# Kernel tuning notes

Measured on AMD Instinct MI355X. Metric: run time of the kernel, lower is better.

The kernel has to match this reference:

```python
import jax, jax.numpy as jnp
import numpy as np

N_HEADS = 16

def setup_inputs() -> dict:
    key = jax.random.key(0)
    ks = jax.random.split(key, 5)
    b, t, k = 2, 2048, 1024
    x = jax.random.normal(ks[0], (b, t, k), dtype=jnp.float32)
    Wq = jax.random.normal(ks[1], (k, k), dtype=jnp.float32) * 0.02
    Wk = jax.random.normal(ks[2], (k, k), dtype=jnp.float32) * 0.02
    Wv = jax.random.normal(ks[3], (k, k), dtype=jnp.float32) * 0.02
    Wo = jax.random.normal(ks[4], (k, k), dtype=jnp.float32) * 0.02
    return {"x": x, "Wq": Wq, "Wk": Wk, "Wv": Wv, "Wo": Wo}

def reference(x, Wq, Wk, Wv, Wo):
    b, t, k = x.shape
    h = N_HEADS
    hs = k // h
    # torch nn.Linear(k, k, bias=False): y = x @ W.T
    Q = (x @ Wq.T).reshape(b, t, h, hs).transpose(0, 2, 1, 3)  # [b,h,t,hs]
    K = (x @ Wk.T).reshape(b, t, h, hs).transpose(0, 2, 1, 3)
    V = (x @ Wv.T).reshape(b, t, h, hs).transpose(0, 2, 1, 3)
    # NOTE: original scales by 1/sqrt(k) (full model dim), not 1/sqrt(hs)
    scores = jnp.einsum('bhqd,bhkd->bhqk', Q, K) / jnp.sqrt(jnp.float32(k))
    causal = jnp.tril(jnp.ones((t, t), dtype=bool))  # [t,t]
    scores = jnp.where(causal[None, None], scores, jnp.float32(-jnp.inf))
    P = jax.nn.softmax(scores, axis=-1)  # [b,h,t,t]
    O = jnp.einsum('bhqk,bhkd->bhqd', P, V)  # [b,h,t,hs]
    O = O.transpose(0, 2, 1, 3).reshape(b, t, k)
    return O @ Wo.T
```

## Files before the change

kernel.cpp:

```cpp
#include <hip/hip_runtime.h>
#include <hip/hip_bf16.h>

typedef __attribute__((ext_vector_type(8))) short bf16x8;
typedef __attribute__((ext_vector_type(4))) float f32x4;
typedef unsigned short u16;
typedef unsigned int u32;

#define MFMA16(a, b, c) __builtin_amdgcn_mfma_f32_16x16x32_bf16((a), (b), (c), 0, 0, 0)

__device__ __forceinline__ void gld16(const void* g, void* l) {
  __builtin_amdgcn_global_load_lds((const __attribute__((address_space(1))) u32*)g,
                                   (__attribute__((address_space(3))) u32*)l, 16, 0, 0);
}

__device__ __forceinline__ u16 f2bf(float f) {
  u32 x = __float_as_uint(f);
  x += 0x7fffu + ((x >> 16) & 1u);
  return (u16)(x >> 16);
}
__device__ __forceinline__ u32 pk2(float lo, float hi) {
  return (u32)f2bf(lo) | ((u32)f2bf(hi) << 16);
}
__device__ __forceinline__ u32 cvtpk(float lo, float hi) {
  u32 r;
  asm("v_cvt_pk_bf16_f32 %0, %1, %2" : "=v"(r) : "v"(lo), "v"(hi));
  return r;
}
__device__ __forceinline__ float exp2a(float x) {
  float r;
  asm("v_exp_f32 %0, %1" : "=v"(r) : "v"(x));
  return r;
}
__device__ __forceinline__ bf16x8 ldfrag(const u16* lds, int row, int kbyte) {
  return *(const bf16x8*)&lds[row * 64 + ((kbyte ^ ((row & 7) << 4)) >> 1)];
}

__global__ __launch_bounds__(256) void cvt_bf16(const float* __restrict__ s, u16* __restrict__ d,
                                                int n4) {
  int i = blockIdx.x * 256 + threadIdx.x;
  if (i < n4) {
    float4 f = ((const float4*)s)[i];
    uint2 o;
    o.x = pk2(f.x, f.y);
    o.y = pk2(f.z, f.w);
    ((uint2*)d)[i] = o;
  }
}

__global__ __launch_bounds__(256) void cvt_all(const float* __restrict__ x,
                                               const float* __restrict__ w0,
                                               const float* __restrict__ w1,
                                               const float* __restrict__ w2,
                                               const float* __restrict__ w3,
                                               u16* __restrict__ xb, u16* __restrict__ d012,
                                               u16* __restrict__ d3) {
  const int bid = blockIdx.x;
  const float* s;
  u16* d;
  int i;
  if (bid < 4096) {
    s = x;
    d = xb;
    i = bid * 256 + threadIdx.x;
  } else {
    const int y = (bid - 4096) >> 10;
    s = (y == 0) ? w0 : (y == 1) ? w1 : (y == 2) ? w2 : w3;
    d = (y == 3) ? d3 : d012 + (size_t)y * 1024 * 1024;
    i = ((bid - 4096) & 1023) * 256 + threadIdx.x;
  }
  float4 f = ((const float4*)s)[i];
  uint2 o;
  o.x = pk2(f.x, f.y);
  o.y = pk2(f.z, f.w);
  ((uint2*)d)[i] = o;
}

template <int MODE, bool BBF, int BM>
__global__ __launch_bounds__(256, 5) void gemm4(const u16* __restrict__ Ab,
                                                const float* __restrict__ W0,
                                                const float* __restrict__ W1,
                                                const float* __restrict__ W2,
                                                const u16* __restrict__ Bb, u16* __restrict__ Cq,
                                                u16* __restrict__ Ck, u16* __restrict__ Cvt,
                                                float* __restrict__ Cf) {
  constexpr int MI = BM / 32;
  __shared__ u16 Alds[BM * 64];
  __shared__ u16 Blds[128 * 64];
  const int tid = threadIdx.x, wid = tid >> 6, lane = tid & 63;
  const int lg = lane >> 4, lr = lane & 15;
  const int wr = wid >> 1, wc = wid & 1;
  const int bid = blockIdx.x;
  const int xcd = bid & 7, slot = bid >> 3;
  int bm, bn;
  if constexpr (MODE == 0) {
    bn = xcd * 3 + (slot % 3);
    bm = slot / 3;
  } else {
    bn = xcd;
    bm = slot;
  }
  const int ng = bn * 128;

  const float* Bf = nullptr;
  const u16* Bbr = nullptr;
  if constexpr (BBF) {
    Bbr = Bb + (size_t)ng * 1024;
  } else {
    if constexpr (MODE == 0)
      Bf = (ng < 1024 ? W0 : (ng < 2048 ? W1 : W2)) + (size_t)(ng & 1023) * 1024;
    else
      Bf = W0 + (size_t)ng * 1024;
  }

  f32x4 acc[MI][4];
#pragma unroll
  for (int i = 0; i < MI; ++i)
#pragma unroll
    for (int j = 0; j < 4; ++j) acc[i][j] = {0.f, 0.f, 0.f, 0.f};

  const u16* Ag0 = Ab + (size_t)(bm * BM) * 1024;
  const int srow8 = lane >> 3, schunk = lane & 7;
  const int brow = tid >> 1, bhalf = tid & 1;
  const u32 stv0 = (u32)(wid * 8 + srow8) * 2048 + (u32)(schunk ^ srow8) * 16;
  const u32 ldsd0 = (u32)(wid * 8) * 128;

  for (int kt = 0; kt < 16; ++kt) {
    __syncthreads();
    {
      const char* At = (const char*)Ag0 + (size_t)kt * 128;
#pragma unroll
      for (int c = 0; c < BM / 32; ++c)
        gld16(At + stv0 + c * 65536, (char*)Alds + ldsd0 + c * 4096);
    }
    if constexpr (BBF) {
      const char* Bt = (const char*)Bbr + (size_t)kt * 128;
#pragma unroll
      for (int c = 0; c < 4; ++c)
        gld16(Bt + stv0 + c * 65536, (char*)Blds + ldsd0 + c * 4096);
    } else {
      const float* s = Bf + (size_t)brow * 1024 + kt * 64 + bhalf * 32;
#pragma unroll
      for (int q = 0; q < 4; ++q) {
        float4 f0 = ((const float4*)s)[2 * q];
        float4 f1 = ((const float4*)s)[2 * q + 1];
        uint4 w;
        w.x = pk2(f0.x, f0.y);
        w.y = pk2(f0.z, f0.w);
        w.z = pk2(f1.x, f1.y);
        w.w = pk2(f1.z, f1.w);
        int ch = (bhalf * 4 + q) ^ (brow & 7);
        *(uint4*)&Blds[brow * 64 + ch * 8] = w;
      }
    }
    __syncthreads();

#pragma unroll
    for (int ks = 0; ks < 2; ++ks) {
      bf16x8 af[MI], bfr[4];
#pragma unroll
      for (int mi = 0; mi < MI; ++mi)
        af[mi] = ldfrag(Alds, wr * (BM / 2) + mi * 16 + lr, ks * 64 + lg * 16);
#pragma unroll
      for (int ni = 0; ni < 4; ++ni) bfr[ni] = ldfrag(Blds, wc * 64 + ni * 16 + lr, ks * 64 + lg * 16);
#pragma unroll
      for (int mi = 0; mi < MI; ++mi)
#pragma unroll
        for (int ni = 0; ni < 4; ++ni) acc[mi][ni] = MFMA16(af[mi], bfr[ni], acc[mi][ni]);
    }
  }

  if constexpr (MODE == 1) {
#pragma unroll
    for (int mi = 0; mi < MI; ++mi)
#pragma unroll
      for (int r = 0; r < 4; ++r) {
        int m = bm * BM + wr * (BM / 2) + mi * 16 + lg * 4 + r;
#pragma unroll
        for (int ni = 0; ni < 4; ++ni)
          Cf[(size_t)m * 1024 + ng + wc * 64 + ni * 16 + lr] = acc[mi][ni][r];
      }
  } else if (ng < 2048) {
    u16* C = (ng < 1024) ? Cq : Ck;
    const float qs = (ng < 1024) ? 0.0450842200f : 1.0f;
    const int nb = ng & 1023;
#pragma unroll
    for (int mi = 0; mi < MI; ++mi)
#pragma unroll
      for (int r = 0; r < 4; ++r) {
        int m = bm * BM + wr * (BM / 2) + mi * 16 + lg * 4 + r;
#pragma unroll
        for (int ni = 0; ni < 4; ++ni)
          C[(size_t)m * 1024 + nb + wc * 64 + ni * 16 + lr] = f2bf(acc[mi][ni][r] * qs);
      }
  } else {
    const int bnum = (bm * BM) >> 11;
    const int nvb = (ng - 2048) + wc * 64;
#pragma unroll
    for (int mi = 0; mi < MI; ++mi) {
      int tb = ((bm * BM) & 2047) + wr * (BM / 2) + mi * 16 + lg * 4;
#pragma unroll
      for (int ni = 0; ni < 4; ++ni) {
        int nv = nvb + ni * 16 + lr;
        ushort4 st;
        st.x = f2bf(acc[mi][ni][0]);
        st.y = f2bf(acc[mi][ni][1]);
        st.z = f2bf(acc[mi][ni][2]);
        st.w = f2bf(acc[mi][ni][3]);
        *(ushort4*)&Cvt[((size_t)(bnum << 10) + nv) * 2048 + tb] = st;
      }
    }
  }
}

__global__ __launch_bounds__(256, 4) void flashD(const u16* __restrict__ Qb,
                                                 const u16* __restrict__ Kb,
                                                 const u16* __restrict__ Vt,
                                                 u16* __restrict__ Ob, u16* __restrict__ accP,
                                                 float* __restrict__ lP) {
  __shared__ u16 Klds[2][64 * 64];
  __shared__ u16 Vlds[2][64 * 64];
  __shared__ u16 Plds[4][16 * 64];
  const int tid = threadIdx.x, wid = tid >> 6, lane = tid & 63;
  const int lg = lane >> 4, lr = lane & 15;
  const int bid = blockIdx.x;
  const int xcd = bid & 7;
  const int slot = bid >> 3;
  int g, jq;
  bool typeY;
  if (slot < 64) {
    g = slot >> 4;
    jq = 16 + (slot & 15);
    typeY = false;
  } else {
    int idx = slot - 64;
    int len = 16 - (idx >> 3);
    int j = idx & 7;
    g = j & 3;
    typeY = (j >> 2) != 0;
    jq = typeY ? (15 + len) : (len - 1);
  }
  const int hb = xcd * 4 + g;
  const int hh = hb & 15, bb = hb >> 4;
  const int q0 = jq * 64;
  const int t0 = typeY ? 16 : 0;
  const int t1 = (!typeY && jq >= 16) ? 16 : (jq + 1);
  const size_t baseqk = ((size_t)bb * 2048) * 1024 + hh * 64;
  const int srow8 = lane >> 3, schunk = lane & 7, ch = schunk ^ srow8;

  const u32 kvo0 = (u32)(wid * 8 + srow8) * 2048 + ch * 16;
  const u32 kvo1 = kvo0 + 32 * 2048;
  const u32 vvo0 = (u32)(wid * 8 + srow8) * 4096 + ch * 16;
  const u32 vvo1 = vvo0 + 32 * 4096;
  const char* Kgp = (const char*)(Kb + baseqk);
  const char* Vgp = (const char*)(Vt + ((size_t)(bb * 1024 + hh * 64)) * 2048);
  const u32 ldsr0 = (u32)(wid * 8) * 128;
  const u32 ldsr1 = ldsr0 + 4096;

  const u32 swzb = (u32)(lr & 7) << 4;
  const char* kfb0 = (const char*)Klds + lr * 128 + ((lg * 16) ^ swzb);
  const char* kfb1 = (const char*)Klds + lr * 128 + ((64 + lg * 16) ^ swzb);
  const char* vfb0 = (const char*)Vlds + lr * 128 + ((lg * 16) ^ swzb);
  const char* vfb1 = (const char*)Vlds + lr * 128 + ((64 + lg * 16) ^ swzb);
  u16* Pw = &Plds[wid][0];
  const int pswz = (lr & 7) << 3;
  const char* pr0 = (const char*)Pw + lr * 128 + (((lg * 8) ^ pswz) * 2);
  const char* pr1 = (const char*)Pw + lr * 128 + (((32 + lg * 8) ^ pswz) * 2);

  bf16x8 qf[2];
  {
    const u16* qp = Qb + baseqk + (size_t)(q0 + wid * 16 + lr) * 1024 + lg * 8;
    qf[0] = *(const bf16x8*)qp;
    qf[1] = *(const bf16x8*)(qp + 32);
  }
  f32x4 acc[4];
#pragma unroll
  for (int dt = 0; dt < 4; ++dt) acc[dt] = {0.f, 0.f, 0.f, 0.f};
  float l_r = 0.f;
  const int qrow = q0 + wid * 16 + lr;

#define STAGE(BUF, KT)                                                  \
  do {                                                                  \
    const char* Kt_ = Kgp + (size_t)(KT) * 131072;                      \
    const char* Vt_ = Vgp + (size_t)(KT) * 128;                         \
    gld16(Kt_ + kvo0, (char*)Klds + (BUF) * 8192 + ldsr0);              \
    gld16(Kt_ + kvo1, (char*)Klds + (BUF) * 8192 + ldsr1);              \
    gld16(Vt_ + vvo0, (char*)Vlds + (BUF) * 8192 + ldsr0);              \
    gld16(Vt_ + vvo1, (char*)Vlds + (BUF) * 8192 + ldsr1);              \
  } while (0)

#define FTILE(BUF, T)                                                            \
  do {                                                                           \
    const int t_ = (T);                                                          \
    if (t_ + 1 < t1) STAGE((BUF) ^ 1, t_ + 1);                                   \
    f32x4 s[4];                                                                  \
    _Pragma("unroll") for (int ni = 0; ni < 4; ++ni) s[ni] = {0.f, 0.f, 0.f, 0.f}; \
    __builtin_amdgcn_s_setprio(1);                                               \
    _Pragma("unroll") for (int ni = 0; ni < 4; ++ni) {                           \
      bf16x8 kb = *(const bf16x8*)(kfb0 + (BUF) * 8192 + ni * 2048);             \
      s[ni] = MFMA16(kb, qf[0], s[ni]);                                          \
    }                                                                            \
    _Pragma("unroll") for (int ni = 0; ni < 4; ++ni) {                           \
      bf16x8 kb = *(const bf16x8*)(kfb1 + (BUF) * 8192 + ni * 2048);             \
      s[ni] = MFMA16(kb, qf[1], s[ni]);                                          \
    }                                                                            \
    __builtin_amdgcn_s_setprio(0);                                               \
    float p[4][4];                                                               \
    float rs = 0.f;                                                              \
    const int kv0_ = t_ * 64;                                                    \
    if (t_ == jq) {                                                              \
      _Pragma("unroll") for (int ni = 0; ni < 4; ++ni)                           \
      _Pragma("unroll") for (int r = 0; r < 4; ++r) {                            \
        float v = s[ni][r];                                                      \
        if (kv0_ + ni * 16 + lg * 4 + r > qrow) v = -1e30f;                      \
        v = exp2a(v);                                                            \
        p[ni][r] = v;                                                            \
        rs += v;                                                                 \
      }                                                                          \
    } else {                                                                     \
      _Pragma("unroll") for (int ni = 0; ni < 4; ++ni)                           \
      _Pragma("unroll") for (int r = 0; r < 4; ++r) {                            \
        float v = exp2a(s[ni][r]);                                               \
        p[ni][r] = v;                                                            \
        rs += v;                                                                 \
      }                                                                          \
    }                                                                            \
    l_r += rs;                                                                   \
    _Pragma("unroll") for (int ni = 0; ni < 4; ++ni) {                           \
      _Pragma("unroll") for (int h = 0; h < 2; ++h) {                            \
        u32 w = cvtpk(p[ni][2 * h], p[ni][2 * h + 1]);                           \
        int col = (ni * 16 + lg * 4 + 2 * h) ^ pswz;                             \
        *(u32*)((char*)Pw + lr * 128 + col * 2) = w;                             \
      }                                                                          \
    }                                                                            \
    bf16x8 pb0 = *(const bf16x8*)pr0;                                            \
    bf16x8 pb1 = *(const bf16x8*)pr1;                                            \
    __builtin_amdgcn_s_setprio(1);                                               \
    _Pragma("unroll") for (int dt = 0; dt < 4; ++dt) {                           \
      bf16x8 a0 = *(const bf16x8*)(vfb0 + (BUF) * 8192 + dt * 2048);             \
      bf16x8 a1 = *(const bf16x8*)(vfb1 + (BUF) * 8192 + dt * 2048);             \
      acc[dt] = MFMA16(a0, pb0, acc[dt]);                                        \
      acc[dt] = MFMA16(a1, pb1, acc[dt]);                                        \
    }                                                                            \
    __builtin_amdgcn_s_setprio(0);                                               \
    __syncthreads();                                                             \
  } while (0)

  STAGE(0, t0);
  __syncthreads();
  int t = t0;
  for (; t + 2 <= t1; t += 2) {
    FTILE(0, t);
    FTILE(1, t + 1);
  }
  if (t < t1) FTILE(0, t);

#undef STAGE
#undef FTILE

  if (!typeY && jq < 16) {
    l_r += __shfl_xor(l_r, 16);
    l_r += __shfl_xor(l_r, 32);
    float inv = 1.f / l_r;
    u16* orow = Ob + baseqk + (size_t)qrow * 1024 + lg * 4;
#pragma unroll
    for (int dt = 0; dt < 4; ++dt) {
      ushort4 st;
      st.x = f2bf(acc[dt][0] * inv);
      st.y = f2bf(acc[dt][1] * inv);
      st.z = f2bf(acc[dt][2] * inv);
      st.w = f2bf(acc[dt][3] * inv);
      *(ushort4*)&orow[dt * 16] = st;
    }
  } else {
    const int p = (typeY ? 512 : 0) + hb * 16 + (jq - 16);
    u16* pp = accP + (size_t)p * 4096 + (size_t)(wid * 16 + lr) * 64 + lg * 4;
#pragma unroll
    for (int dt = 0; dt < 4; ++dt) {
      ushort4 st;
      st.x = f2bf(acc[dt][0]);
      st.y = f2bf(acc[dt][1]);
      st.z = f2bf(acc[dt][2]);
      st.w = f2bf(acc[dt][3]);
      *(ushort4*)&pp[dt * 16] = st;
    }
    l_r += __shfl_xor(l_r, 16);
    l_r += __shfl_xor(l_r, 32);
    if (lg == 0) lP[p * 64 + wid * 16 + lr] = l_r;
  }
}

__global__ __launch_bounds__(256) void fcomb(const u16* __restrict__ accP,
                                             const float* __restrict__ lP,
                                             u16* __restrict__ Ob) {
  const int pid = blockIdx.x, tid = threadIdx.x;
  const int hb = pid >> 4, jq = 16 + (pid & 15);
  const int bb = hb >> 4, hh = hb & 15;
  const int row = tid >> 2, dseg = (tid & 3) << 4;
  const u16* a0 = accP + (size_t)pid * 4096 + row * 64 + dseg;
  const u16* a1 = accP + (size_t)(pid + 512) * 4096 + row * 64 + dseg;
  float inv = 1.f / (lP[pid * 64 + row] + lP[(pid + 512) * 64 + row]);
  u16 b0[16], b1[16], ov[16];
  *(uint4*)&b0[0] = ((const uint4*)a0)[0];
  *(uint4*)&b0[8] = ((const uint4*)a0)[1];
  *(uint4*)&b1[0] = ((const uint4*)a1)[0];
  *(uint4*)&b1[8] = ((const uint4*)a1)[1];
#pragma unroll
  for (int i = 0; i < 16; ++i) {
    float f = __uint_as_float((u32)b0[i] << 16) + __uint_as_float((u32)b1[i] << 16);
    ov[i] = f2bf(f * inv);
  }
  u16* od = Ob + (size_t)bb * 2048 * 1024 + (size_t)(jq * 64 + row) * 1024 + hh * 64 + dseg;
  ((uint4*)od)[0] = *(uint4*)&ov[0];
  ((uint4*)od)[1] = *(uint4*)&ov[8];
}

extern "C" void kernel_launch(void* const* d_in, const int* in_sizes, int n_in, void* d_out,
                              int out_size, void* d_ws, size_t ws_size, hipStream_t stream) {
  const float* x = (const float*)d_in[0];
  const float* Wq = (const float*)d_in[1];
  const float* Wk = (const float*)d_in[2];
  const float* Wv = (const float*)d_in[3];
  const float* Wo = (const float*)d_in[4];
  float* out = (float*)d_out;

  u16* xb = (u16*)d_ws;
  u16* Qb = xb + (size_t)4096 * 1024;
  u16* Kb = Qb + (size_t)4096 * 1024;
  u16* Vt = Kb + (size_t)4096 * 1024;
  u16* Ob = Qb;
  u16* Wb = Vt + (size_t)4096 * 1024;
  u16* Wob = Wb + (size_t)3072 * 1024;
  u16* accP = xb;

  const bool full = ws_size >= ((size_t)40 << 20);
  float* lP = full ? (float*)Wb : (float*)(Vt + (size_t)4096 * 1024);

  if (full) {
    cvt_all<<<8192, 256, 0, stream>>>(x, Wq, Wk, Wv, Wo, xb, Wb, Wob);
    gemm4<0, true, 64><<<1536, 256, 0, stream>>>(xb, nullptr, nullptr, nullptr, Wb, Qb, Kb, Vt,
                                                 nullptr);
    flashD<<<1536, 256, 0, stream>>>(Qb, Kb, Vt, Ob, accP, lP);
    fcomb<<<512, 256, 0, stream>>>(accP, lP, Ob);
    gemm4<1, true, 64><<<512, 256, 0, stream>>>(Ob, nullptr, nullptr, nullptr, Wob, nullptr,
                                                nullptr, nullptr, out);
  } else {
    cvt_bf16<<<4096, 256, 0, stream>>>(x, xb, 4096 * 1024 / 4);
    gemm4<0, false, 64><<<1536, 256, 0, stream>>>(xb, Wq, Wk, Wv, nullptr, Qb, Kb, Vt, nullptr);
    flashD<<<1536, 256, 0, stream>>>(Qb, Kb, Vt, Ob, accP, lP);
    fcomb<<<512, 256, 0, stream>>>(accP, lP, Ob);
    gemm4<1, false, 64><<<512, 256, 0, stream>>>(Ob, Wo, nullptr, nullptr, nullptr, nullptr,
                                                 nullptr, nullptr, out);
  }
}
```

Baseline: 102.6 us.

## Halve flash attention KV tile to 32 rows to raise occupancy

The flash attention kernel now processes 32-key sub-tiles instead of 64, halving the K/V/P shared-memory buffers and changing the swizzle and staging layout to match. Launch bounds rise from 4 to 6 blocks per SIMD to allow more resident waves for latency hiding. In exchange it doubles the number of barriers and loop iterations per query tile and shrinks the MFMA work between synchronisations. The P buffer is padded to a 40-element stride instead of XOR swizzled.

```diff
diff --git a/kernel.cpp b/kernel.cpp
--- a/kernel.cpp
+++ b/kernel.cpp
@@ -212,14 +212,14 @@
   }
 }
 
-__global__ __launch_bounds__(256, 4) void flashD(const u16* __restrict__ Qb,
+__global__ __launch_bounds__(256, 6) void flashE(const u16* __restrict__ Qb,
                                                  const u16* __restrict__ Kb,
                                                  const u16* __restrict__ Vt,
                                                  u16* __restrict__ Ob, u16* __restrict__ accP,
                                                  float* __restrict__ lP) {
-  __shared__ u16 Klds[2][64 * 64];
-  __shared__ u16 Vlds[2][64 * 64];
-  __shared__ u16 Plds[4][16 * 64];
+  __shared__ u16 Klds[2][32 * 64];
+  __shared__ u16 Vlds[2][64 * 32];
+  __shared__ u16 Plds[4][16 * 40];
   const int tid = threadIdx.x, wid = tid >> 6, lane = tid & 63;
   const int lg = lane >> 4, lr = lane & 15;
   const int bid = blockIdx.x;
@@ -244,27 +244,23 @@
   const int q0 = jq * 64;
   const int t0 = typeY ? 16 : 0;
   const int t1 = (!typeY && jq >= 16) ? 16 : (jq + 1);
+  const int tt1 = 2 * t1;
   const size_t baseqk = ((size_t)bb * 2048) * 1024 + hh * 64;
-  const int srow8 = lane >> 3, schunk = lane & 7, ch = schunk ^ srow8;
-
-  const u32 kvo0 = (u32)(wid * 8 + srow8) * 2048 + ch * 16;
-  const u32 kvo1 = kvo0 + 32 * 2048;
-  const u32 vvo0 = (u32)(wid * 8 + srow8) * 4096 + ch * 16;
-  const u32 vvo1 = vvo0 + 32 * 4096;
+
+  const int krow = wid * 8 + (lane >> 3);
+  const u32 kvoK = (u32)krow * 2048 + (u32)((lane & 7) ^ (krow & 7)) * 16;
+  const int vrow = wid * 16 + (lane >> 2);
+  const u32 kvoV = (u32)vrow * 4096 + (u32)((lane & 3) ^ (vrow & 3)) * 16;
   const char* Kgp = (const char*)(Kb + baseqk);
   const char* Vgp = (const char*)(Vt + ((size_t)(bb * 1024 + hh * 64)) * 2048);
-  const u32 ldsr0 = (u32)(wid * 8) * 128;
-  const u32 ldsr1 = ldsr0 + 4096;
-
-  const u32 swzb = (u32)(lr & 7) << 4;
-  const char* kfb0 = (const char*)Klds + lr * 128 + ((lg * 16) ^ swzb);
-  const char* kfb1 = (const char*)Klds + lr * 128 + ((64 + lg * 16) ^ swzb);
-  const char* vfb0 = (const char*)Vlds + lr * 128 + ((lg * 16) ^ swzb);
-  const char* vfb1 = (const char*)Vlds + lr * 128 + ((64 + lg * 16) ^ swzb);
+  const u32 ldsw = (u32)wid * 1024;
+
+  const u32 kswz = (u32)(lr & 7) << 4;
+  const char* kfb0 = (const char*)Klds + lr * 128 + ((lg * 16) ^ kswz);
+  const char* kfb1 = (const char*)Klds + lr * 128 + ((64 + lg * 16) ^ kswz);
+  const char* vfb = (const char*)Vlds + lr * 64 + ((lg * 16) ^ ((u32)(lr & 3) << 4));
   u16* Pw = &Plds[wid][0];
-  const int pswz = (lr & 7) << 3;
-  const char* pr0 = (const char*)Pw + lr * 128 + (((lg * 8) ^ pswz) * 2);
-  const char* pr1 = (const char*)Pw + lr * 128 + (((32 + lg * 8) ^ pswz) * 2);
+  const char* prd = (const char*)Pw + lr * 80 + lg * 16;
 
   bf16x8 qf[2];
   {
@@ -278,81 +274,75 @@
   float l_r = 0.f;
   const int qrow = q0 + wid * 16 + lr;
 
-#define STAGE(BUF, KT)                                                  \
-  do {                                                                  \
-    const char* Kt_ = Kgp + (size_t)(KT) * 131072;                      \
-    const char* Vt_ = Vgp + (size_t)(KT) * 128;                         \
-    gld16(Kt_ + kvo0, (char*)Klds + (BUF) * 8192 + ldsr0);              \
-    gld16(Kt_ + kvo1, (char*)Klds + (BUF) * 8192 + ldsr1);              \
-    gld16(Vt_ + vvo0, (char*)Vlds + (BUF) * 8192 + ldsr0);              \
-    gld16(Vt_ + vvo1, (char*)Vlds + (BUF) * 8192 + ldsr1);              \
+#define STAGE(BUF, TT)                                                   \
+  do {                                                                   \
+    gld16(Kgp + (size_t)(TT) * 65536 + kvoK,                             \
+          (char*)Klds + (BUF) * 4096 + ldsw);                            \
+    gld16(Vgp + (size_t)(TT) * 64 + kvoV,                                \
+          (char*)Vlds + (BUF) * 4096 + ldsw);                            \
   } while (0)
 
-#define FTILE(BUF, T)                                                            \
-  do {                                                                           \
-    const int t_ = (T);                                                          \
-    if (t_ + 1 < t1) STAGE((BUF) ^ 1, t_ + 1);                                   \
-    f32x4 s[4];                                                                  \
-    _Pragma("unroll") for (int ni = 0; ni < 4; ++ni) s[ni] = {0.f, 0.f, 0.f, 0.f}; \
-    __builtin_amdgcn_s_setprio(1);                                               \
-    _Pragma("unroll") for (int ni = 0; ni < 4; ++ni) {                           \
-      bf16x8 kb = *(const bf16x8*)(kfb0 + (BUF) * 8192 + ni * 2048);             \
-      s[ni] = MFMA16(kb, qf[0], s[ni]);                                          \
-    }                                                                            \
-    _Pragma("unroll") for (int ni = 0; ni < 4; ++ni) {                           \
-      bf16x8 kb = *(const bf16x8*)(kfb1 + (BUF) * 8192 + ni * 2048);             \
-      s[ni] = MFMA16(kb, qf[1], s[ni]);                                          \
-    }                                                                            \
-    __builtin_amdgcn_s_setprio(0);                                               \
-    float p[4][4];                                                               \
-    float rs = 0.f;                                                              \
-    const int kv0_ = t_ * 64;                                                    \
-    if (t_ == jq) {                                                              \
-      _Pragma("unroll") for (int ni = 0; ni < 4; ++ni)                           \
-      _Pragma("unroll") for (int r = 0; r < 4; ++r) {                            \
-        float v = s[ni][r];                                                      \
-        if (kv0_ + ni * 16 + lg * 4 + r > qrow) v = -1e30f;                      \
-        v = exp2a(v);                                                            \
-        p[ni][r] = v;                                                            \
-        rs += v;                                                                 \
-      }                                                                          \
-    } else {                                                                     \
-      _Pragma("unroll") for (int ni = 0; ni < 4; ++ni)                           \
-      _Pragma("unroll") for (int r = 0; r < 4; ++r) {                            \
-        float v = exp2a(s[ni][r]);                                               \
-        p[ni][r] = v;                                                            \
-        rs += v;                                                                 \
-      }                                                                          \
-    }                                                                            \
-    l_r += rs;                                                                   \
-    _Pragma("unroll") for (int ni = 0; ni < 4; ++ni) {                           \
-      _Pragma("unroll") for (int h = 0; h < 2; ++h) {                            \
-        u32 w = cvtpk(p[ni][2 * h], p[ni][2 * h + 1]);                           \
-        int col = (ni * 16 + lg * 4 + 2 * h) ^ pswz;                             \
-        *(u32*)((char*)Pw + lr * 128 + col * 2) = w;                             \
-      }                                                                          \
-    }                                                                            \
-    bf16x8 pb0 = *(const bf16x8*)pr0;                                            \
-    bf16x8 pb1 = *(const bf16x8*)pr1;                                            \
-    __builtin_amdgcn_s_setprio(1);                                               \
-    _Pragma("unroll") for (int dt = 0; dt < 4; ++dt) {                           \
-      bf16x8 a0 = *(const bf16x8*)(vfb0 + (BUF) * 8192 + dt * 2048);             \
-      bf16x8 a1 = *(const bf16x8*)(vfb1 + (BUF) * 8192 + dt * 2048);             \
-      acc[dt] = MFMA16(a0, pb0, acc[dt]);                                        \
-      acc[dt] = MFMA16(a1, pb1, acc[dt]);                                        \
-    }                                                                            \
-    __builtin_amdgcn_s_setprio(0);                                               \
-    __syncthreads();                                                             \
+#define FTILE(BUF, TT)                                                             \
+  do {                                                                             \
+    const int tt_ = (TT);                                                          \
+    if (tt_ + 1 < tt1) STAGE((BUF) ^ 1, tt_ + 1);                                  \
+    f32x4 s[2];                                                                    \
+    s[0] = {0.f, 0.f, 0.f, 0.f};                                                   \
+    s[1] = {0.f, 0.f, 0.f, 0.f};                                                   \
+    __builtin_amdgcn_s_setprio(1);                                                 \
+    _Pragma("unroll") for (int ni = 0; ni < 2; ++ni) {                             \
+      bf16x8 k0 = *(const bf16x8*)(kfb0 + (BUF) * 4096 + ni * 2048);               \
+      bf16x8 k1 = *(const bf16x8*)(kfb1 + (BUF) * 4096 + ni * 2048);               \
+      s[ni] = MFMA16(k0, qf[0], s[ni]);                                            \
+      s[ni] = MFMA16(k1, qf[1], s[ni]);                                            \
+    }                                                                              \
+    __builtin_amdgcn_s_setprio(0);                                                 \
+    float p[2][4];                                                                 \
+    float rs = 0.f;                                                                \
+    const int kv0_ = tt_ * 32;                                                     \
+    if ((tt_ >> 1) == jq) {                                                        \
+      _Pragma("unroll") for (int ni = 0; ni < 2; ++ni)                             \
+      _Pragma("unroll") for (int r = 0; r < 4; ++r) {                              \
+        float v = s[ni][r];                                                        \
+        if (kv0_ + ni * 16 + lg * 4 + r > qrow) v = -1e30f;                        \
+        v = exp2a(v);                                                              \
+        p[ni][r] = v;                                                              \
+        rs += v;                                                                   \
+      }                                                                            \
+    } else {                                                                       \
+      _Pragma("unroll") for (int ni = 0; ni < 2; ++ni)                             \
+      _Pragma("unroll") for (int r = 0; r < 4; ++r) {                              \
+        float v = exp2a(s[ni][r]);                                                 \
+        p[ni][r] = v;                                                              \
+        rs += v;                                                                   \
+      }                                                                            \
+    }                                                                              \
+    l_r += rs;                                                                     \
+    _Pragma("unroll") for (int ni = 0; ni < 2; ++ni) {                             \
+      _Pragma("unroll") for (int h = 0; h < 2; ++h) {                              \
+        u32 w = cvtpk(p[ni][2 * h], p[ni][2 * h + 1]);                             \
+        *(u32*)((char*)Pw + lr * 80 + (ni * 16 + lg * 4 + 2 * h) * 2) = w;         \
+      }                                                                            \
+    }                                                                              \
+    bf16x8 pb = *(const bf16x8*)prd;                                               \
+    __builtin_amdgcn_s_setprio(1);                                                 \
+    _Pragma("unroll") for (int dt = 0; dt < 4; ++dt) {                             \
+      bf16x8 a0 = *(const bf16x8*)(vfb + (BUF) * 4096 + dt * 1024);                \
+      acc[dt] = MFMA16(a0, pb, acc[dt]);                                           \
+    }                                                                              \
+    __builtin_amdgcn_s_setprio(0);                                                 \
+    __syncthreads();                                                               \
   } while (0)
 
-  STAGE(0, t0);
+  const int tt0 = 2 * t0;
+  STAGE(0, tt0);
   __syncthreads();
-  int t = t0;
-  for (; t + 2 <= t1; t += 2) {
-    FTILE(0, t);
-    FTILE(1, t + 1);
-  }
-  if (t < t1) FTILE(0, t);
+  int tt = tt0;
+  for (; tt + 2 <= tt1; tt += 2) {
+    FTILE(0, tt);
+    FTILE(1, tt + 1);
+  }
+  if (tt < tt1) FTILE(0, tt);
 
 #undef STAGE
 #undef FTILE
@@ -439,14 +429,14 @@
     cvt_all<<<8192, 256, 0, stream>>>(x, Wq, Wk, Wv, Wo, xb, Wb, Wob);
     gemm4<0, true, 64><<<1536, 256, 0, stream>>>(xb, nullptr, nullptr, nullptr, Wb, Qb, Kb, Vt,
                                                  nullptr);
-    flashD<<<1536, 256, 0, stream>>>(Qb, Kb, Vt, Ob, accP, lP);
+    flashE<<<1536, 256, 0, stream>>>(Qb, Kb, Vt, Ob, accP, lP);
     fcomb<<<512, 256, 0, stream>>>(accP, lP, Ob);
     gemm4<1, true, 64><<<512, 256, 0, stream>>>(Ob, nullptr, nullptr, nullptr, Wob, nullptr,
                                                 nullptr, nullptr, out);
   } else {
     cvt_bf16<<<4096, 256, 0, stream>>>(x, xb, 4096 * 1024 / 4);
     gemm4<0, false, 64><<<1536, 256, 0, stream>>>(xb, Wq, Wk, Wv, nullptr, Qb, Kb, Vt, nullptr);
-    flashD<<<1536, 256, 0, stream>>>(Qb, Kb, Vt, Ob, accP, lP);
+    flashE<<<1536, 256, 0, stream>>>(Qb, Kb, Vt, Ob, accP, lP);
     fcomb<<<512, 256, 0, stream>>>(accP, lP, Ob);
     gemm4<1, false, 64><<<512, 256, 0, stream>>>(Ob, Wo, nullptr, nullptr, nullptr, nullptr,
                                                  nullptr, nullptr, out);
```

After: 103.3 us. No clear change (+0.7%).
